# Kernel optimization log

Measured on AMD Instinct MI355X. Metric: run time of the kernel, lower is better.

## Reference

```python
import jax, jax.numpy as jnp
import numpy as np

C, BS1, NODE, L, K = 2, 9, 820, 3, 17  # BS1 = 1 + bs
SQRT2 = 1.4142135623730951
SQRT2PI = 2.5066282746310002
EPS = 1e-30  # fp32-safe stand-in for the 1e-307 used in the float64 original

# Gauss-Hermite quadrature points (physicists'), as in gausshermite(k, dims=[1,1,1,1,-1])
_x, _ = np.polynomial.hermite.hermgauss(K)
_XN = _x.reshape(1, 1, 1, 1, K).astype(np.float32)
_mi, _mj = np.meshgrid(_x, _x)
_XI = _mi.reshape(1, 1, 1, 1, K * K).astype(np.float32)
_XJ = _mj.reshape(1, 1, 1, 1, K * K).astype(np.float32)

# fine-to-coarse MRF edge target indices (length 819), exact tile/reshape pattern from __init__
_id1 = np.tile(np.tile(np.arange(729, 810).reshape(-1, 1), (1, 3)).reshape(-1, 1, 27), (1, 3, 1)).reshape(-1)
_id2 = np.tile(np.tile(np.arange(810, 819).reshape(-1, 1), (1, 3)).reshape(-1, 9), (1, 3)).reshape(-1)
_ID = np.concatenate([_id1, _id2, np.full(9, 819)]).astype(np.int32)


def setup_inputs() -> dict:
    key = jax.random.key(0)
    k1, k2, k3 = jax.random.split(key, 3)
    mu = jax.random.normal(k1, (C, BS1, NODE, L, 1), jnp.float32)
    sigma = jax.random.uniform(k2, (C, BS1, NODE, L, 1), jnp.float32, minval=0.1, maxval=1.0)
    w = jax.random.normal(k3, (C, BS1, 1, L, 1), jnp.float32)
    return {"mu": mu, "sigma": sigma, "w": w}


def reference(mu, sigma, w):
    xq = jnp.asarray(_XN)
    xi = jnp.asarray(_XI)
    xj = jnp.asarray(_XJ)
    ids = jnp.asarray(_ID)

    # quadrature points aligned with each mixture component's distribution
    xn = xq * sigma * SQRT2 + mu                         # (C,BS1,820,L,K)
    u1, o1 = mu[:, :, :-1], sigma[:, :, :-1]             # (C,BS1,819,L,1)
    u2, o2 = mu[:, :, ids], sigma[:, :, ids]             # gather along node axis
    x1 = xi * o1 * SQRT2 + u1                            # (C,BS1,819,L,K*K)
    x2 = xj * o2 * SQRT2 + u2
    xe = jnp.stack([x1, x2], -1)                         # (C,BS1,819,L,K*K,2)

    alpha = jax.nn.softmax(w, axis=3)                    # (C,BS1,1,L,1)
    alf = alpha[:, :, :, None]                           # (C,BS1,1,1,L,1)

    # node log marginal: mixture density at each quadrature point
    o = sigma[:, :, :, None]                             # (C,BS1,820,1,L,1)
    pn = jnp.exp(-((xn[:, :, :, :, None, :] - mu[:, :, :, None]) / o) ** 2 / 2) / (o * SQRT2PI)
    lpn = jnp.log(jnp.sum(pn * alf, 4) + EPS)            # (C,BS1,820,L,K)
    lpn = jnp.concatenate([
        jnp.concatenate([lpn[:, :1, :729], jnp.zeros_like(lpn[:, 1:, :729])], 1),
        lpn[:, :, 729:]], 2)

    # edge log marginal (product of per-endpoint densities, mixture-weighted)
    o1_, o2_ = o1[:, :, :, None], o2[:, :, :, None]      # (C,BS1,819,1,L,1)
    b1 = jnp.exp(-((x1[:, :, :, :, None, :] - u1[:, :, :, None]) / o1_) ** 2 / 2) / (o1_ * SQRT2PI)
    b1 = jnp.concatenate([
        jnp.concatenate([b1[:, :1, :729], jnp.ones_like(b1[:, 1:, :729])], 1),
        b1[:, :, 729:]], 2)
    b2 = jnp.exp(-((x2[:, :, :, :, None, :] - u2[:, :, :, None]) / o2_) ** 2 / 2) / (o2_ * SQRT2PI)
    lpe = jnp.log(jnp.sum(b1 * b2 * alf, 4) + EPS)       # (C,BS1,819,L,K*K)

    return xn, xe, lpn, lpe, alpha, o1, o2
```

## Files before the change

kernel.cpp:

```cpp
#include <hip/hip_runtime.h>

#define NC    2
#define NB    9
#define NNODE 820
#define NL    3
#define NK    17
#define G     8
#define NGB   103

#define EPSF     1e-30f
#define C_SCF    0.84932178f
#define KLPN     0.46971920f
#define KE       0.22063560f

#define OFF_XN    0LL
#define OFF_XE    752760LL
#define OFF_LPN   26315388LL
#define OFF_LPE   27068148LL
#define OFF_ALPHA 39849462LL
#define OFF_O1    39849516LL
#define OFF_O2    39893742LL

constexpr double csqrt(double v) {
    if (v <= 0.0) return 0.0;
    double y = v > 1.0 ? v : 1.0;
    for (int i = 0; i < 80; ++i) y = 0.5 * (y + v / y);
    return y;
}

struct HNodesF { float x[NK]; };

constexpr HNodesF compute_nodes() {
    const int n = NK;
    const double PIM4 = 0.7511255444649425;
    double c1[NK + 1] = {}, c2[NK + 1] = {};
    for (int j = 1; j <= n; ++j) {
        c1[j] = csqrt(2.0 / (double)j);
        c2[j] = csqrt(((double)j - 1.0) / (double)j);
    }
    const double PPC = csqrt(2.0 * (double)n);
    double xr[9] = {};
    double z = 0.0;
    for (int i = 0; i < 9; ++i) {
        if (i == 0)      z = csqrt(2.0 * n + 1.0) - 1.85575 * 0.552905;
        else if (i == 1) z -= 1.14 * 3.34327 / z;
        else if (i == 2) z = 1.86 * z - 0.86 * xr[0];
        else if (i == 3) z = 1.91 * z - 0.91 * xr[1];
        else             z = 2.0 * z - xr[i - 2];
        for (int it = 0; it < 24; ++it) {
            double p1 = PIM4, p2 = 0.0;
            for (int j = 1; j <= n; ++j) {
                double p3 = p2;
                p2 = p1;
                p1 = z * c1[j] * p2 - c2[j] * p3;
            }
            double pp = PPC * p2;
            double z1 = z;
            z = z1 - p1 / pp;
            double d = z - z1; if (d < 0.0) d = -d;
            if (d <= 3.0e-14) break;
        }
        xr[i] = z;
    }
    HNodesF f{};
    for (int i = 0; i < 9; ++i) {
        f.x[16 - i] = (float)xr[i];
        f.x[i]      = (float)(-xr[i]);
    }
    return f;
}

struct TabF { float v[289 * 2]; };
constexpr TabF make_tab() {
    HNodesF h = compute_nodes();
    TabF t{};
    for (int q = 0; q < 289; ++q) {
        t.v[2 * q]     = (float)((double)h.x[q % 17] * 1.4142135623730951);
        t.v[2 * q + 1] = (float)((double)h.x[q / 17] * 1.4142135623730951);
    }
    return t;
}
constexpr TabF TABC = make_tab();

__device__ __forceinline__ int idOf(int n) {
    if (n < 729) { return 729 + (n / 81) * 9 + (n % 27) / 3; }
    if (n < 810) { int m = n - 729; return 810 + (m / 27) * 3 + (m % 9) / 3; }
    return 819;
}

__device__ __forceinline__ float rcpf(float x) { return __builtin_amdgcn_rcpf(x); }

__device__ __forceinline__ float sel3(float a0, float a1, float a2, int i) {
    float r = a0;
    r = (i == 1) ? a1 : r;
    r = (i == 2) ? a2 : r;
    return r;
}

__global__ __launch_bounds__(256) void fused_kernel(const float* __restrict__ mu,
                                                    const float* __restrict__ sg,
                                                    const float* __restrict__ w,
                                                    float* __restrict__ out) {
    const int g   = blockIdx.x;
    const int cb  = blockIdx.y;
    const int b   = cb % NB;
    const int n0  = g * G;
    const int tid = threadIdx.x;

    __shared__ float2 tab[289];
    __shared__ float  params[96];
    __shared__ float  sCEj[1224];
    __shared__ float  sEi [1224];
    __shared__ float  sLpj[408];

    {
        const float2* tc = (const float2*)TABC.v;
        tab[tid] = tc[tid];
        if (tid < 33) tab[256 + tid] = tc[256 + tid];
    }

    const size_t cbase = (size_t)cb * NNODE;

    if (tid < 96) {
        int nn = tid / 12, r = tid - nn * 12;
        int n = n0 + nn;
        if (n > 819) n = 819;
        size_t b1a = (cbase + n) * 3;
        size_t b2a = (cbase + (size_t)idOf(n)) * 3;
        float v;
        if (r < 3)      v = mu[b1a + r];
        else if (r < 6) v = sg[b1a + r - 3];
        else if (r < 9) v = mu[b2a + r - 6];
        else            v = sg[b2a + r - 9];
        params[tid] = v;
    }

    const float* wB = w + cb * 3;
    float w0 = wB[0], w1 = wB[1], w2 = wB[2];
    float wm = fmaxf(w0, fmaxf(w1, w2));
    float e0 = __expf(w0 - wm), e1 = __expf(w1 - wm), e2 = __expf(w2 - wm);
    float ainv = 1.0f / (e0 + e1 + e2);
    float a0 = e0 * ainv, a1 = e1 * ainv, a2 = e2 * ainv;

    __syncthreads();

    for (int v = tid; v < 1224; v += 256) {
        int s  = v / 51, r = v - s * 51;
        int m  = r / 17, j = r - m * 17;
        int nn = s / 3,  l1 = s - nn * 3;
        int n  = n0 + nn;
        const float* P = params + nn * 12;
        float u1l = P[l1],     s1l = P[3 + l1];
        float u2l = P[6 + l1], s2l = P[9 + l1];
        float u1m = P[m],      s1m = P[3 + m];
        float u2m = P[6 + m],  s2m = P[9 + m];
        float i2m = C_SCF * rcpf(s2m);
        float i1m = C_SCF * rcpf(s1m);
        float am  = sel3(a0, a1, a2, m);
        bool  mk  = (b >= 1) && (n < 729);
        float cm  = mk ? (am * i2m * KLPN) : (am * i1m * i2m * KE);
        float xv  = tab[j].x;
        float x2j = fmaf(xv, s2l, u2l);
        float d   = (x2j - u2m) * i2m;
        sCEj[v] = cm * exp2f(-(d * d));
        float x1i = fmaf(xv, s1l, u1l);
        float f   = (x1i - u1m) * i1m;
        sEi[v]  = exp2f(-(f * f));
    }
    __syncthreads();
    for (int t = tid; t < 408; t += 256) {
        int s = t / 17, j = t - s * 17;
        float sum = sCEj[s * 51 + j] + sCEj[s * 51 + 17 + j] + sCEj[s * 51 + 34 + j];
        sLpj[t] = __logf(sum + EPSF);
    }
    __syncthreads();

    const int wv = tid >> 6, ln = tid & 63;
    const int j0 = tid / 17, i0 = tid - 17 * j0;
    const int qt = 256 + ln;
    const int jt = qt / 17, it = qt - 17 * jt;
    const size_t ecb = (size_t)cb * 819;

    for (int nn = 0; nn < G; ++nn) {
        int n = n0 + nn;
        if (n >= 819) break;
        const bool mk = (b >= 1) && (n < 729);
        const float* P = params + nn * 12;
        float2* xp0 = reinterpret_cast<float2*>(out + OFF_XE) + (ecb + n) * 867;
        float*  lp0 = out + OFF_LPE + (ecb + n) * 867;

#pragma unroll
        for (int l1 = 0; l1 < 3; ++l1) {
            const int sec = nn * 3 + l1;
            float u1l = P[l1],     s1l = P[3 + l1];
            float u2l = P[6 + l1], s2l = P[9 + l1];
            float2* xp = xp0 + l1 * 289;
            float*  lp = lp0 + l1 * 289;
            const float* CE = sCEj + sec * 51;
            const float* EI = sEi  + sec * 51;
            const float* LJ = sLpj + sec * 17;

            auto body = [&](int q, int i, int j) {
                float2 tv = tab[q];
                float x1 = fmaf(tv.x, s1l, u1l);
                float x2 = fmaf(tv.y, s2l, u2l);
                xp[q] = make_float2(x1, x2);
                float lv;
                if (mk) {
                    lv = LJ[j];
                } else {
                    float sum = fmaf(EI[i], CE[j],
                                fmaf(EI[17 + i], CE[17 + j],
                                     EI[34 + i] * CE[34 + j]));
                    lv = __logf(sum + EPSF);
                }
                lp[q] = lv;
            };

            body(tid, i0, j0);
            if (wv == (sec & 3) && ln < 33) body(qt, it, jt);
        }
    }

    for (int t = tid; t < G * 51; t += 256) {
        int nn = t / 51;
        int n  = n0 + nn;
        if (n >= 820) break;
        int r  = t - 51 * nn;
        int l1 = r / 17;
        int k  = r - 17 * l1;
        const float* P = params + nn * 12;
        float ul = P[l1], sl = P[3 + l1];
        float xn = fmaf(tab[k].x, sl, ul);
        out[OFF_XN + (cbase + n0) * 51 + t] = xn;

        float lp = 0.0f;
        if (!(b >= 1 && n < 729)) {
            float ia = C_SCF * rcpf(P[3]);
            float ib = C_SCF * rcpf(P[4]);
            float ic = C_SCF * rcpf(P[5]);
            float d0 = (xn - P[0]) * ia;
            float d1 = (xn - P[1]) * ib;
            float d2 = (xn - P[2]) * ic;
            float sum = a0 * ia * exp2f(-(d0 * d0))
                      + a1 * ib * exp2f(-(d1 * d1))
                      + a2 * ic * exp2f(-(d2 * d2));
            lp = __logf(sum * KLPN + EPSF);
        }
        out[OFF_LPN + (cbase + n0) * 51 + t] = lp;
    }

    if (tid < 24) {
        int nn = tid / 3, c = tid - 3 * nn;
        int n = n0 + nn;
        if (n < 819) out[OFF_O1 + (ecb + n) * 3 + c] = params[nn * 12 + 3 + c];
    } else if (tid < 48) {
        int t = tid - 24;
        int nn = t / 3, c = t - 3 * nn;
        int n = n0 + nn;
        if (n < 819) out[OFF_O2 + (ecb + n) * 3 + c] = params[nn * 12 + 9 + c];
    }

    if (g == 0 && cb == 0 && tid >= 64 && tid < 118) {
        int t = tid - 64;
        int cb2 = t / 3, l = t - 3 * cb2;
        const float* wB2 = w + cb2 * 3;
        float v0 = wB2[0], v1 = wB2[1], v2 = wB2[2];
        float vm = fmaxf(v0, fmaxf(v1, v2));
        float f0 = __expf(v0 - vm), f1 = __expf(v1 - vm), f2 = __expf(v2 - vm);
        float finv = 1.0f / (f0 + f1 + f2);
        float fl = (l == 0) ? f0 : ((l == 1) ? f1 : f2);
        out[OFF_ALPHA + t] = fl * finv;
    }
}

extern "C" void kernel_launch(void* const* d_in, const int* in_sizes, int n_in,
                              void* d_out, int out_size, void* d_ws, size_t ws_size,
                              hipStream_t stream) {
    const float* mu    = (const float*)d_in[0];
    const float* sigma = (const float*)d_in[1];
    const float* w     = (const float*)d_in[2];
    float* out = (float*)d_out;

    hipLaunchKernelGGL(fused_kernel, dim3(NGB, NC * NB), dim3(256), 0, stream,
                       mu, sigma, w, out);
}
```

Before: 35.16 us.

## Split xe writes into separate block set from lpe/lpn compute blocks

Blocks are split into two groups. The first writes only the edge quadrature points xe, four nodes per block. The second keeps the log-marginal (lpe, lpn) computation plus xn, o1, o2 and alpha, eight nodes per block. The goal is more blocks and better store bandwidth by separating the large xe write stream from the exp/log work. The cost is a larger grid, a second load of the parameter and table data, and control flow that diverges between the two groups.

```diff
diff --git a/kernel.cpp b/kernel.cpp
--- a/kernel.cpp
+++ b/kernel.cpp
@@ -5,8 +5,10 @@
 #define NNODE 820
 #define NL    3
 #define NK    17
-#define G     8
-#define NGB   103
+#define GA    4
+#define NGA   205
+#define GB    8
+#define NGBB  103
 
 #define EPSF     1e-30f
 #define C_SCF    0.84932178f
@@ -101,11 +103,13 @@
                                                     const float* __restrict__ sg,
                                                     const float* __restrict__ w,
                                                     float* __restrict__ out) {
-    const int g   = blockIdx.x;
+    const int gx  = blockIdx.x;
     const int cb  = blockIdx.y;
     const int b   = cb % NB;
-    const int n0  = g * G;
     const int tid = threadIdx.x;
+    const size_t cbase = (size_t)cb * NNODE;
+    const size_t ecb   = (size_t)cb * 819;
+    const int wv = tid >> 6, ln = tid & 63;
 
     __shared__ float2 tab[289];
     __shared__ float  params[96];
@@ -119,9 +123,51 @@
         if (tid < 33) tab[256 + tid] = tc[256 + tid];
     }
 
-    const size_t cbase = (size_t)cb * NNODE;
-
-    if (tid < 96) {
+    if (gx < NGA) {
+        const int n0 = gx * GA;
+        if (tid < GA * 12) {
+            int nn = tid / 12, r = tid - nn * 12;
+            int n = n0 + nn;
+            size_t b1a = (cbase + n) * 3;
+            size_t b2a = (cbase + (size_t)idOf(n)) * 3;
+            float v;
+            if (r < 3)      v = mu[b1a + r];
+            else if (r < 6) v = sg[b1a + r - 3];
+            else if (r < 9) v = mu[b2a + r - 6];
+            else            v = sg[b2a + r - 9];
+            params[tid] = v;
+        }
+        __syncthreads();
+
+        for (int nn = 0; nn < GA; ++nn) {
+            int n = n0 + nn;
+            if (n >= 819) break;
+            const float* P = params + nn * 12;
+            float2* xp0 = reinterpret_cast<float2*>(out + OFF_XE) + (ecb + n) * 867;
+#pragma unroll
+            for (int l1 = 0; l1 < 3; ++l1) {
+                float u1l = P[l1],     s1l = P[3 + l1];
+                float u2l = P[6 + l1], s2l = P[9 + l1];
+                float2* xp = xp0 + l1 * 289;
+                {
+                    float2 tv = tab[tid];
+                    xp[tid] = make_float2(fmaf(tv.x, s1l, u1l), fmaf(tv.y, s2l, u2l));
+                }
+                const int sec = nn * 3 + l1;
+                if (wv == (sec & 3) && ln < 33) {
+                    int q = 256 + ln;
+                    float2 tv = tab[q];
+                    xp[q] = make_float2(fmaf(tv.x, s1l, u1l), fmaf(tv.y, s2l, u2l));
+                }
+            }
+        }
+        return;
+    }
+
+    const int gb = gx - NGA;
+    const int n0 = gb * GB;
+
+    if (tid < GB * 12) {
         int nn = tid / 12, r = tid - nn * 12;
         int n = n0 + nn;
         if (n > 819) n = 819;
@@ -175,36 +221,25 @@
     }
     __syncthreads();
 
-    const int wv = tid >> 6, ln = tid & 63;
     const int j0 = tid / 17, i0 = tid - 17 * j0;
     const int qt = 256 + ln;
     const int jt = qt / 17, it = qt - 17 * jt;
-    const size_t ecb = (size_t)cb * 819;
-
-    for (int nn = 0; nn < G; ++nn) {
+
+    for (int nn = 0; nn < GB; ++nn) {
         int n = n0 + nn;
         if (n >= 819) break;
         const bool mk = (b >= 1) && (n < 729);
-        const float* P = params + nn * 12;
-        float2* xp0 = reinterpret_cast<float2*>(out + OFF_XE) + (ecb + n) * 867;
-        float*  lp0 = out + OFF_LPE + (ecb + n) * 867;
+        float* lp0 = out + OFF_LPE + (ecb + n) * 867;
 
 #pragma unroll
         for (int l1 = 0; l1 < 3; ++l1) {
             const int sec = nn * 3 + l1;
-            float u1l = P[l1],     s1l = P[3 + l1];
-            float u2l = P[6 + l1], s2l = P[9 + l1];
-            float2* xp = xp0 + l1 * 289;
-            float*  lp = lp0 + l1 * 289;
+            float* lp = lp0 + l1 * 289;
             const float* CE = sCEj + sec * 51;
             const float* EI = sEi  + sec * 51;
             const float* LJ = sLpj + sec * 17;
 
             auto body = [&](int q, int i, int j) {
-                float2 tv = tab[q];
-                float x1 = fmaf(tv.x, s1l, u1l);
-                float x2 = fmaf(tv.y, s2l, u2l);
-                xp[q] = make_float2(x1, x2);
                 float lv;
                 if (mk) {
                     lv = LJ[j];
@@ -222,7 +257,7 @@
         }
     }
 
-    for (int t = tid; t < G * 51; t += 256) {
+    for (int t = tid; t < GB * 51; t += 256) {
         int nn = t / 51;
         int n  = n0 + nn;
         if (n >= 820) break;
@@ -261,7 +296,7 @@
         if (n < 819) out[OFF_O2 + (ecb + n) * 3 + c] = params[nn * 12 + 9 + c];
     }
 
-    if (g == 0 && cb == 0 && tid >= 64 && tid < 118) {
+    if (gb == 0 && cb == 0 && tid >= 64 && tid < 118) {
         int t = tid - 64;
         int cb2 = t / 3, l = t - 3 * cb2;
         const float* wB2 = w + cb2 * 3;
@@ -282,6 +317,6 @@
     const float* w     = (const float*)d_in[2];
     float* out = (float*)d_out;
 
-    hipLaunchKernelGGL(fused_kernel, dim3(NGB, NC * NB), dim3(256), 0, stream,
+    hipLaunchKernelGGL(fused_kernel, dim3(NGA + NGBB, NC * NB), dim3(256), 0, stream,
                        mu, sigma, w, out);
 }
```

Result: faster. 34.35 us (-2.3%).
